# Kernel tuning notes

Hardware: AMD Instinct MI355X
Metric: run time of the kernel (lower is better)

Reference implementation:

```python
import jax, jax.numpy as jnp
import numpy as np

RES = 64
C_DIM = 64
N_BLOCKS = 4
EPS = 1e-12


def conv2d(x, w, b, pad):
    out = jax.lax.conv_general_dilated(
        x, w, window_strides=(1, 1), padding=[(pad, pad), (pad, pad)],
        dimension_numbers=('NCHW', 'OIHW', 'NCHW'))
    return out + b[None, :, None, None]


def unfold3(x):
    # F.unfold(kernel=3, padding=1): [B,C,H,W] -> [B, C*9, H*W], torch ordering (c, ki, kj)
    B, C, H, W = x.shape
    xp = jnp.pad(x, ((0, 0), (0, 0), (1, 1), (1, 1)))
    patches = jnp.stack([xp[:, :, ki:ki + H, kj:kj + W]
                         for ki in range(3) for kj in range(3)], axis=2)  # [B,C,9,H,W]
    return patches.reshape(B, C * 9, H * W)


def fold3(t, H, W):
    # F.fold(kernel=3, padding=1): sum overlapping patches back to [B,C,H,W]
    B, C9, L = t.shape
    C = C9 // 9
    t = t.reshape(B, C, 3, 3, H, W)
    out = jnp.zeros((B, C, H + 2, W + 2), t.dtype)
    for ki in range(3):
        for kj in range(3):
            out = out.at[:, :, ki:ki + H, kj:kj + W].add(t[:, :, ki, kj])
    return out[:, :, 1:H + 1, 1:W + 1]


def setup_inputs() -> dict:
    key = jax.random.key(0)
    ks = jax.random.split(key, 16)
    B, L, C = 4, RES * RES, C_DIM
    s = 0.05
    inp = {
        'c0': jax.random.normal(ks[0], (B, L, C), jnp.float32),
        'f0': jax.random.normal(ks[1], (B, L, C), jnp.float32),
        'c1': jax.random.normal(ks[2], (B, L, C), jnp.float32),
        'head_w': jax.random.normal(ks[3], (C, C, 5, 5), jnp.float32) * s,
        'head_b': jax.random.normal(ks[4], (C,), jnp.float32) * s,
        'rb_w1': jax.random.normal(ks[5], (N_BLOCKS, C, C, 3, 3), jnp.float32) * s,
        'rb_b1': jax.random.normal(ks[6], (N_BLOCKS, C), jnp.float32) * s,
        'rb_w2': jax.random.normal(ks[7], (N_BLOCKS, C, C, 3, 3), jnp.float32) * s,
        'rb_b2': jax.random.normal(ks[8], (N_BLOCKS, C), jnp.float32) * s,
        'tail_w': jax.random.normal(ks[9], (C, C, 5, 5), jnp.float32) * s,
        'tail_b': jax.random.normal(ks[10], (C,), jnp.float32) * s,
        'sq_w': jax.random.normal(ks[11], (C, 2 * C, 5, 5), jnp.float32) * s,
        'sq_b': jax.random.normal(ks[12], (C,), jnp.float32) * s,
    }
    return inp


def reference(c0, f0, c1, head_w, head_b, rb_w1, rb_b1, rb_w2, rb_b2,
              tail_w, tail_b, sq_w, sq_b):
    B, L, C = c1.shape
    H = W = RES
    c1 = c1.swapaxes(1, 2).reshape(B, C, H, W)
    c0 = c0.swapaxes(1, 2).reshape(B, C, H, W)
    f0 = f0.swapaxes(1, 2).reshape(B, C, H, W)
    Delta_c = c1 - c0

    # --- search_Trans: patch correlation + best-match texture transfer ---
    c1u = unfold3(c1)                       # [B, C9, L]
    c0u = unfold3(c0).swapaxes(1, 2)        # [B, L, C9]
    c0n = c0u / jnp.maximum(jnp.linalg.norm(c0u, axis=2, keepdims=True), EPS)
    c1n = c1u / jnp.maximum(jnp.linalg.norm(c1u, axis=1, keepdims=True), EPS)
    R = jnp.einsum('blk,bkm->blm', c0n, c1n)  # [B, L, L]
    R_star = jnp.max(R, axis=1)               # [B, L]
    R_arg = jnp.argmax(R, axis=1)              # [B, L]
    f0u = unfold3(f0)                          # [B, C9, L]
    Tu = jnp.take_along_axis(f0u, R_arg[:, None, :], axis=2)
    T = fold3(Tu, H, W) / 9.0                  # [B, C, H, W]
    S = R_star.reshape(B, 1, H, W)

    # --- residual conv stack on Delta_c ---
    x1 = conv2d(Delta_c, head_w, head_b, 2)
    x = x1
    for i in range(rb_w1.shape[0]):  # NOTE: original feeds x1 into every block
        h = jax.nn.relu(conv2d(x1, rb_w1[i], rb_b1[i], 1))
        x = conv2d(h, rb_w2[i], rb_b2[i], 1) + x1
    x = conv2d(x, tail_w, tail_b, 2)
    Delta_c_fea = x + x1

    x = conv2d(jnp.concatenate([Delta_c_fea, T], axis=1), sq_w, sq_b, 2)
    out = Delta_c_fea + x * S
    return out.reshape(B, C, L).swapaxes(1, 2)
```

## Files before the change

### kernel.cpp

```cpp
#include <hip/hip_runtime.h>
#include <hip/hip_bf16.h>


#define BATCH 4

typedef unsigned short u16;
typedef unsigned int   u32;
typedef __attribute__((ext_vector_type(8))) short short8;
typedef __attribute__((ext_vector_type(4))) float f32x4;

__device__ __forceinline__ void bsplit2(float a, float b, u32& ho, u32& lo) {
  __hip_bfloat16 ha = __float2bfloat16(a), hb = __float2bfloat16(b);
  float ra = a - __bfloat162float(ha), rb = b - __bfloat162float(hb);
  __hip_bfloat16 la = __float2bfloat16(ra), lb = __float2bfloat16(rb);
  ho = (u32)*(u16*)&ha | ((u32)*(u16*)&hb << 16);
  lo = (u32)*(u16*)&la | ((u32)*(u16*)&lb << 16);
}

__device__ __forceinline__ void gload_lds16(const void* g, void* l) {
  __builtin_amdgcn_global_load_lds((const __attribute__((address_space(1))) void*)g,
                                   (__attribute__((address_space(3))) void*)l, 16, 0, 0);
}

__global__ __launch_bounds__(256) void split_pad_kernel(const float* __restrict__ c0,
    const float* __restrict__ c1, u16* __restrict__ p0h, u16* __restrict__ p0l,
    u16* __restrict__ p1h, u16* __restrict__ p1l,
    float* __restrict__ ss0, float* __restrict__ ss1)
{
  int b = blockIdx.y, t = threadIdx.x;
  int pix = blockIdx.x * 4 + (t >> 6);
  int c = t & 63;
  int py = pix / 66, px = pix - py * 66;
  size_t d = ((size_t)b * 4356 + pix) * 64 + c;
  bool interior = (py >= 1 && py <= 64 && px >= 1 && px <= 64);
  float v0 = 0.f, v1 = 0.f;
  if (interior) {
    size_t s = (((size_t)b << 12) + ((py - 1) << 6) + (px - 1)) * 64 + c;
    v0 = c0[s]; v1 = c1[s];
  }
  __hip_bfloat16 h = __float2bfloat16(v0);
  float r = v0 - __bfloat162float(h);
  __hip_bfloat16 lo = __float2bfloat16(r);
  p0h[d] = *(u16*)&h; p0l[d] = *(u16*)&lo;
  h = __float2bfloat16(v1);
  r = v1 - __bfloat162float(h);
  lo = __float2bfloat16(r);
  p1h[d] = *(u16*)&h; p1l[d] = *(u16*)&lo;
  float s0 = v0 * v0, s1 = v1 * v1;
#pragma unroll
  for (int off = 32; off; off >>= 1) {
    s0 += __shfl_xor(s0, off);
    s1 += __shfl_xor(s1, off);
  }
  if (c == 0 && interior) {
    int sstid = (b << 12) + ((py - 1) << 6) + (px - 1);
    ss0[sstid] = s0;
    ss1[sstid] = s1;
  }
}

__global__ __launch_bounds__(256) void wprep_all(
    const float* __restrict__ hw, u16* __restrict__ whh, u16* __restrict__ whl,
    const float* __restrict__ r1, u16* __restrict__ w1h, u16* __restrict__ w1l,
    const float* __restrict__ r2, u16* __restrict__ w2h, u16* __restrict__ w2l,
    const float* __restrict__ tw, u16* __restrict__ wth, u16* __restrict__ wtl,
    const float* __restrict__ sw, u16* __restrict__ wsh, u16* __restrict__ wsl,
    const float* __restrict__ ss0, float* __restrict__ inv0)
{
  int bid = blockIdx.x;
  if (bid >= 1888) {
    int tid = (bid - 1888) * 256 + threadIdx.x;
    int b = tid >> 12, l = tid & 4095;
    int y = l >> 6, x = l & 63;
    const float* ssb = ss0 + (b << 12);
    float s = 0.f;
    for (int dy = -1; dy <= 1; ++dy) {
      int yy = y + dy; if ((unsigned)yy >= 64u) continue;
      for (int dx = -1; dx <= 1; ++dx) {
        int xx = x + dx; if ((unsigned)xx >= 64u) continue;
        s += ssb[(yy << 6) + xx];
      }
    }
    inv0[tid] = 1.f / fmaxf(sqrtf(s), 1e-12f);
    return;
  }
  const float* src; u16 *wh, *wl; int Cin, KK, n, i;
  if (bid < 400)       { src = hw; wh = whh; wl = whl; Cin = 64;  KK = 25; n = 102400; i = bid * 256; }
  else if (bid < 544)  { src = r1; wh = w1h; wl = w1l; Cin = 64;  KK = 9;  n = 36864;  i = (bid - 400) * 256; }
  else if (bid < 688)  { src = r2; wh = w2h; wl = w2l; Cin = 64;  KK = 9;  n = 36864;  i = (bid - 544) * 256; }
  else if (bid < 1088) { src = tw; wh = wth; wl = wtl; Cin = 64;  KK = 25; n = 102400; i = (bid - 688) * 256; }
  else                 { src = sw; wh = wsh; wl = wsl; Cin = 128; KK = 25; n = 204800; i = (bid - 1088) * 256; }
  i += threadIdx.x;
  if (i >= n) return;
  int per = Cin * KK;
  int cout = i / per;
  int rem = i - cout * per;
  int cin = rem / KK;
  int tap = rem - cin * KK;
  float x = src[i];
  __hip_bfloat16 h = __float2bfloat16(x);
  float r = x - __bfloat162float(h);
  __hip_bfloat16 lo = __float2bfloat16(r);
  int d = (tap * 64 + cout) * Cin + cin;
  wh[d] = *(u16*)&h;
  wl[d] = *(u16*)&lo;
}

__global__ __launch_bounds__(512) void corr_mfma(const u16* __restrict__ p0h,
    const u16* __restrict__ p0l, const u16* __restrict__ p1h, const u16* __restrict__ p1l,
    const float* __restrict__ inv0, float* __restrict__ pval, int* __restrict__ pidx)
{
  __shared__ __align__(16) u16 smem[32768];
  int mt = blockIdx.x, lt = blockIdx.y, b = blockIdx.z;
  int t = threadIdx.x;
  int lane = t & 63, w = t >> 6;
  int wa = w >> 1, wm = w & 1;
  int mat = w >> 1, half = w & 1;
  int cc = lane & 15, q = lane >> 4;
  const size_t boff = (size_t)b * 278784;
  const u16* msrc = (mat == 0) ? p0h : (mat == 1) ? p0l : (mat == 2) ? p1h : p1l;
  msrc += boff;
  const float* inv0b = inv0 + (b << 12);
  int isB = mat >> 1;

  int srow0 = lane >> 2;
  int cs_g  = (lane & 3) ^ ((lane >> 3) & 3);
  int sw    = (cc >> 1) & 3;

  const u16* gb[4];
#pragma unroll
  for (int ii = 0; ii < 4; ++ii) {
    int k = ((half * 4 + ii) << 4) + srow0;
    gb[ii] = msrc + ((((k >> 6) * 66) + (k & 63)) << 6) + (cs_g << 3);
  }

  auto stage = [&](int ssub, int sph, u16* dstbase) {
    int r = sph >> 1, hh = sph & 1;
    int ki = r / 3, kj = r - ki * 3;
    int pbr = isB ? (mt << 1) : ((lt << 3) + (ssub << 1));
    int uoff = (((pbr + ki) * 66 + kj) << 6) + (hh << 5);
#pragma unroll
    for (int ii = 0; ii < 4; ++ii)
      gload_lds16(gb[ii] + uoff, dstbase + ((half * 4 + ii) << 9));
  };

  float bval[4] = {-1e30f, -1e30f, -1e30f, -1e30f};
  int   bidx[4] = {0, 0, 0, 0};

  stage(0, 0, smem + (mat << 12));

  for (int sub = 0; sub < 4; ++sub) {
    int row0 = (lt << 9) + (sub << 7);
    f32x4 acc[2][4];
#pragma unroll
    for (int i = 0; i < 2; ++i)
#pragma unroll
      for (int j = 0; j < 4; ++j) acc[i][j] = (f32x4){0.f, 0.f, 0.f, 0.f};

    for (int ph = 0; ph < 18; ++ph) {
      int g = sub * 18 + ph;
      int nxt = g + 1;
      if (nxt < 72) {
        int np = ph + 1, ns = sub;
        if (np == 18) { np = 0; ++ns; }
        stage(ns, np, smem + ((nxt & 1) << 14) + (mat << 12));
        asm volatile("s_waitcnt vmcnt(4)" ::: "memory");
      } else {
        asm volatile("s_waitcnt vmcnt(0)" ::: "memory");
      }
      __builtin_amdgcn_s_barrier();
      __builtin_amdgcn_sched_barrier(0);
      const u16* bb = smem + ((g & 1) << 14);
      short8 afh[2], afl[2], bfh[4], bfl[4];
#pragma unroll
      for (int i = 0; i < 2; ++i) {
        int ra = (((wa << 5) + (i << 4) + cc) << 5) + ((q ^ sw) << 3);
        afh[i] = *(const short8*)(&bb[ra]);
        afl[i] = *(const short8*)(&bb[4096 + ra]);
      }
#pragma unroll
      for (int j = 0; j < 2; ++j) {
        int rb = (((wm << 6) + (j << 4) + cc) << 5) + ((q ^ sw) << 3);
        bfh[j] = *(const short8*)(&bb[8192 + rb]);
        bfl[j] = *(const short8*)(&bb[12288 + rb]);
      }
      __builtin_amdgcn_s_setprio(1);
#pragma unroll
      for (int j = 0; j < 4; ++j) {
        if (j < 2) {
          int rb = (((wm << 6) + ((j + 2) << 4) + cc) << 5) + ((q ^ sw) << 3);
          bfh[j + 2] = *(const short8*)(&bb[8192 + rb]);
          bfl[j + 2] = *(const short8*)(&bb[12288 + rb]);
        }
        __builtin_amdgcn_sched_barrier(0);
        acc[0][j] = __builtin_amdgcn_mfma_f32_16x16x32_bf16(afh[0], bfl[j], acc[0][j], 0, 0, 0);
        acc[0][j] = __builtin_amdgcn_mfma_f32_16x16x32_bf16(afl[0], bfh[j], acc[0][j], 0, 0, 0);
        acc[0][j] = __builtin_amdgcn_mfma_f32_16x16x32_bf16(afh[0], bfh[j], acc[0][j], 0, 0, 0);
        acc[1][j] = __builtin_amdgcn_mfma_f32_16x16x32_bf16(afh[1], bfl[j], acc[1][j], 0, 0, 0);
        acc[1][j] = __builtin_amdgcn_mfma_f32_16x16x32_bf16(afl[1], bfh[j], acc[1][j], 0, 0, 0);
        acc[1][j] = __builtin_amdgcn_mfma_f32_16x16x32_bf16(afh[1], bfh[j], acc[1][j], 0, 0, 0);
        __builtin_amdgcn_sched_barrier(0);
      }
      __builtin_amdgcn_s_setprio(0);
      __builtin_amdgcn_sched_barrier(0);
      __builtin_amdgcn_s_barrier();
    }
#pragma unroll
    for (int i = 0; i < 2; ++i) {
#pragma unroll
      for (int rg = 0; rg < 4; ++rg) {
        int l = row0 + (wa << 5) + (i << 4) + (q << 2) + rg;
        float sc = inv0b[l];
#pragma unroll
        for (int j = 0; j < 4; ++j) {
          float v = acc[i][j][rg] * sc;
          if (v > bval[j]) { bval[j] = v; bidx[j] = l; }
        }
      }
    }
  }

  __syncthreads();
  float* lval = (float*)smem;
  int*   lidx = (int*)((char*)smem + 8192);
  int slot = (wa << 2) + q;
#pragma unroll
  for (int j = 0; j < 4; ++j) {
    int col = (wm << 6) + (j << 4) + cc;
    lval[col * 16 + slot] = bval[j];
    lidx[col * 16 + slot] = bidx[j];
  }
  __syncthreads();
  if (t < 128) {
    float bv = -1e30f; int bi = 0x7FFFFFFF;
    for (int s = 0; s < 16; ++s) {
      float v = lval[t * 16 + s]; int id = lidx[t * 16 + s];
      if (v > bv || (v == bv && id < bi)) { bv = v; bi = id; }
    }
    size_t o = (size_t)(((b << 3) + lt) << 12) + (mt << 7) + t;
    pval[o] = bv; pidx[o] = bi;
  }
}

__global__ __launch_bounds__(256) void tgather_kernel(const float* __restrict__ f0,
    const float* __restrict__ pval, const int* __restrict__ pidx,
    const float* __restrict__ ss1, float* __restrict__ S, float* __restrict__ T)
{
  __shared__ int a3[192];
  int y = blockIdx.x, b = blockIdx.y, t = threadIdx.x;
  if (t < 192) {
    int r = t >> 6, xx = t & 63;
    int yy = y + r - 1;
    bool ok = (yy >= 0 && yy < 64);
    float bv = -1e30f; int bi = 0x7FFFFFFF;
    if (ok) {
      int m = (yy << 6) + xx;
      for (int ltv = 0; ltv < 8; ++ltv) {
        size_t o = (size_t)(((b << 3) + ltv) << 12) + m;
        float v = pval[o]; int id = pidx[o];
        if (v > bv || (v == bv && id < bi)) { bv = v; bi = id; }
      }
      if (r == 1) {
        const float* ssb = ss1 + (b << 12);
        float s = 0.f;
        for (int dy = -1; dy <= 1; ++dy) {
          int y2 = yy + dy; if ((unsigned)y2 >= 64u) continue;
          for (int dx = -1; dx <= 1; ++dx) {
            int x2 = xx + dx; if ((unsigned)x2 >= 64u) continue;
            s += ssb[(y2 << 6) + x2];
          }
        }
        S[(b << 12) + m] = bv / fmaxf(sqrtf(s), 1e-12f);
      }
    }
    a3[t] = (ok && (unsigned)bi < 4096u) ? bi : 0;
  }
  __syncthreads();
  int c = t & 63, pg = t >> 6;
  for (int it = 0; it < 16; ++it) {
    int px = pg + (it << 2);
    float sum = 0.f;
#pragma unroll
    for (int ki = 0; ki < 3; ++ki) {
      int yn = y + 1 - ki;
      if (yn < 0 || yn >= 64) continue;
#pragma unroll
      for (int kj = 0; kj < 3; ++kj) {
        int xn = px + 1 - kj;
        if (xn < 0 || xn >= 64) continue;
        int p = a3[((2 - ki) << 6) + xn];
        int sy = (p >> 6) + ki - 1, sx = (p & 63) + kj - 1;
        if (sy >= 0 && sy < 64 && sx >= 0 && sx < 64)
          sum += f0[((((size_t)b << 12) + (sy << 6) + sx) << 6) + c];
      }
    }
    T[((((size_t)b << 12) + (y << 6) + px)) * 64 + c] = sum * (1.f / 9.f);
  }
}

template<int KS, int CINCH>
__global__ __launch_bounds__(256) void conv_mfma(const float* __restrict__ in0,
    const float* __restrict__ in1, const u16* __restrict__ whp, const u16* __restrict__ wlp,
    const float* __restrict__ bias, float* __restrict__ outp,
    const float* __restrict__ res, const float* __restrict__ smul, int dorelu, int dm)
{
  constexpr int P = KS / 2;
  constexpr int CIN = CINCH * 32;
  constexpr int NKH = CINCH / 2;
  constexpr int NIT = KS * KS * NKH;
  constexpr int AST = 72;
  __shared__ __align__(16) u16 Ah[2][32 * AST], Al[2][32 * AST];
  __shared__ __align__(16) u16 Bh[2][64 * AST], Bl[2][64 * AST];
  int tile = blockIdx.x, b = blockIdx.y;
  int t = threadIdx.x;
  int lane = t & 63, w = t >> 6;
  int wpx = w >> 1, wm = w & 1;
  int cc = lane & 15, q = lane >> 4;
  int ty = tile >> 1, txb = (tile & 1) << 5;
  const size_t abase = (size_t)b << 12;
  f32x4 acc[2];
  acc[0] = (f32x4){0.f, 0.f, 0.f, 0.f};
  acc[1] = (f32x4){0.f, 0.f, 0.f, 0.f};

  uint4 rg[8];
  int arow = t >> 2, acs = t & 3;
  int tb = t - 128;
  int brow = tb >> 1, bhalf = tb & 1;

  auto issue_loads = [&](int itn) {
    int tapn = (NKH == 1) ? itn : (itn >> 1);
    int kh   = (NKH == 1) ? 0 : (itn & 1);
    int ki = tapn / KS, kj = tapn - ki * KS;
    if (t < 128) {
#pragma unroll
      for (int k = 0; k < 8; ++k) rg[k] = make_uint4(0u, 0u, 0u, 0u);
      int iy = ty + ki - P;
      int ix = txb + arow + kj - P;
      if ((unsigned)iy < 64u && (unsigned)ix < 64u) {
        size_t base = (abase + (iy << 6) + ix) << 6;
        int cg = kh * 64 + acs * 16;
        if (dm) {
#pragma unroll
          for (int k = 0; k < 4; ++k) {
            rg[k]     = *(const uint4*)(in0 + base + cg + 4 * k);
            rg[4 + k] = *(const uint4*)(in1 + base + cg + 4 * k);
          }
        } else {
          const float* sp = (CINCH == 4 && kh == 1) ? (in1 + base + (cg - 64))
                                                    : (in0 + base + cg);
#pragma unroll
          for (int k = 0; k < 4; ++k) rg[k] = *(const uint4*)(sp + 4 * k);
        }
      }
    } else {
      size_t so = (size_t)(tapn * 64 + brow) * CIN + kh * 64 + bhalf * 32;
#pragma unroll
      for (int k = 0; k < 4; ++k) {
        rg[k]     = *(const uint4*)&whp[so + 8 * k];
        rg[4 + k] = *(const uint4*)&wlp[so + 8 * k];
      }
    }
  };

  auto write_lds = [&](int cur) {
    if (t < 128) {
      float v[16];
      if (dm) {
#pragma unroll
        for (int k = 0; k < 4; ++k)
#pragma unroll
          for (int e = 0; e < 4; ++e)
            v[k * 4 + e] = __uint_as_float((&rg[4 + k].x)[e]) - __uint_as_float((&rg[k].x)[e]);
      } else {
#pragma unroll
        for (int k = 0; k < 4; ++k)
#pragma unroll
          for (int e = 0; e < 4; ++e)
            v[k * 4 + e] = __uint_as_float((&rg[k].x)[e]);
      }
      uint4 uh0, ul0, uh1, ul1;
      bsplit2(v[0], v[1], uh0.x, ul0.x);
      bsplit2(v[2], v[3], uh0.y, ul0.y);
      bsplit2(v[4], v[5], uh0.z, ul0.z);
      bsplit2(v[6], v[7], uh0.w, ul0.w);
      bsplit2(v[8], v[9], uh1.x, ul1.x);
      bsplit2(v[10], v[11], uh1.y, ul1.y);
      bsplit2(v[12], v[13], uh1.z, ul1.z);
      bsplit2(v[14], v[15], uh1.w, ul1.w);
      int o = arow * AST + acs * 16;
      *(uint4*)&Ah[cur][o]     = uh0;
      *(uint4*)&Ah[cur][o + 8] = uh1;
      *(uint4*)&Al[cur][o]     = ul0;
      *(uint4*)&Al[cur][o + 8] = ul1;
    } else {
      int o = brow * AST + bhalf * 32;
#pragma unroll
      for (int k = 0; k < 4; ++k) {
        *(uint4*)&Bh[cur][o + 8 * k] = rg[k];
        *(uint4*)&Bl[cur][o + 8 * k] = rg[4 + k];
      }
    }
  };

  issue_loads(0);
  for (int it = 0; it < NIT; ++it) {
    int cur = it & 1;
    write_lds(cur);
    if (it + 1 < NIT) issue_loads(it + 1);
    asm volatile("s_waitcnt lgkmcnt(0)" ::: "memory");
    __builtin_amdgcn_s_barrier();
    __builtin_amdgcn_sched_barrier(0);
    short8 afh[2], afl[2], bfh[2][2], bfl[2][2];
#pragma unroll
    for (int ks = 0; ks < 2; ++ks) {
      int ra = ((wpx << 4) + cc) * AST + ks * 32 + (q << 3);
      afh[ks] = *(const short8*)&Ah[cur][ra];
      afl[ks] = *(const short8*)&Al[cur][ra];
#pragma unroll
      for (int j = 0; j < 2; ++j) {
        int rb = ((wm << 5) + (j << 4) + cc) * AST + ks * 32 + (q << 3);
        bfh[j][ks] = *(const short8*)&Bh[cur][rb];
        bfl[j][ks] = *(const short8*)&Bl[cur][rb];
      }
    }
#pragma unroll
    for (int ks = 0; ks < 2; ++ks) {
      acc[0] = __builtin_amdgcn_mfma_f32_16x16x32_bf16(afh[ks], bfl[0][ks], acc[0], 0, 0, 0);
      acc[1] = __builtin_amdgcn_mfma_f32_16x16x32_bf16(afh[ks], bfl[1][ks], acc[1], 0, 0, 0);
      acc[0] = __builtin_amdgcn_mfma_f32_16x16x32_bf16(afl[ks], bfh[0][ks], acc[0], 0, 0, 0);
      acc[1] = __builtin_amdgcn_mfma_f32_16x16x32_bf16(afl[ks], bfh[1][ks], acc[1], 0, 0, 0);
      acc[0] = __builtin_amdgcn_mfma_f32_16x16x32_bf16(afh[ks], bfh[0][ks], acc[0], 0, 0, 0);
      acc[1] = __builtin_amdgcn_mfma_f32_16x16x32_bf16(afh[ks], bfh[1][ks], acc[1], 0, 0, 0);
    }
  }
#pragma unroll
  for (int rgi = 0; rgi < 4; ++rgi) {
    int p = (ty << 6) + txb + (wpx << 4) + (q << 2) + rgi;
#pragma unroll
    for (int j = 0; j < 2; ++j) {
      int cout = (wm << 5) + (j << 4) + cc;
      float v = acc[j][rgi] + bias[cout];
      if (dorelu) v = fmaxf(v, 0.f);
      size_t oi = ((abase + p) << 6) + cout;
      if (smul) v = res[oi] + v * smul[abase + p];
      else if (res) v += res[oi];
      outp[oi] = v;
    }
  }
}

extern "C" void kernel_launch(void* const* d_in, const int* in_sizes, int n_in,
                              void* d_out, int out_size, void* d_ws, size_t ws_size,
                              hipStream_t stream)
{
  (void)in_sizes; (void)n_in; (void)out_size; (void)ws_size;
  const float* c0     = (const float*)d_in[0];
  const float* f0     = (const float*)d_in[1];
  const float* c1     = (const float*)d_in[2];
  const float* head_w = (const float*)d_in[3];
  const float* head_b = (const float*)d_in[4];
  const float* rb_w1  = (const float*)d_in[5];
  const float* rb_b1  = (const float*)d_in[6];
  const float* rb_w2  = (const float*)d_in[7];
  const float* rb_b2  = (const float*)d_in[8];
  const float* tail_w = (const float*)d_in[9];
  const float* tail_b = (const float*)d_in[10];
  const float* sq_w   = (const float*)d_in[11];
  const float* sq_b   = (const float*)d_in[12];
  float* out = (float*)d_out;
  char* ws = (char*)d_ws;

  const size_t OFF_SS0  = 0;
  const size_t OFF_SS1  = 65536;
  const size_t OFF_INV0 = 131072;
  const size_t OFF_S    = 262144;
  const size_t OFF_PVAL = 393216;
  const size_t OFF_PIDX = 917504;
  const size_t OFF_WHH  = 1441792;
  const size_t OFF_WHL  = 1646592;
  const size_t OFF_W1H  = 1851392;
  const size_t OFF_W1L  = 1925120;
  const size_t OFF_W2H  = 1998848;
  const size_t OFF_W2L  = 2072576;
  const size_t OFF_WTH  = 2146304;
  const size_t OFF_WTL  = 2351104;
  const size_t OFF_WSH  = 2555904;
  const size_t OFF_WSL  = 2965504;
  const size_t OFF_P0H  = 3375104;
  const size_t OFF_P0L  = OFF_P0H + 2230272;
  const size_t OFF_P1H  = OFF_P0L + 2230272;
  const size_t OFF_P1L  = OFF_P1H + 2230272;
  const size_t OFF_SA   = 3375104;
  const size_t OFF_SB   = 7569408;
  const size_t OFF_SC   = 11763712;

  float* ss0  = (float*)(ws + OFF_SS0);
  float* ss1  = (float*)(ws + OFF_SS1);
  float* inv0 = (float*)(ws + OFF_INV0);
  float* Sbuf = (float*)(ws + OFF_S);
  float* pval = (float*)(ws + OFF_PVAL);
  int*   pidx = (int*)(ws + OFF_PIDX);
  u16* whh = (u16*)(ws + OFF_WHH); u16* whl = (u16*)(ws + OFF_WHL);
  u16* w1h = (u16*)(ws + OFF_W1H); u16* w1l = (u16*)(ws + OFF_W1L);
  u16* w2h = (u16*)(ws + OFF_W2H); u16* w2l = (u16*)(ws + OFF_W2L);
  u16* wth = (u16*)(ws + OFF_WTH); u16* wtl = (u16*)(ws + OFF_WTL);
  u16* wsh = (u16*)(ws + OFF_WSH); u16* wsl = (u16*)(ws + OFF_WSL);
  u16* p0h = (u16*)(ws + OFF_P0H); u16* p0l = (u16*)(ws + OFF_P0L);
  u16* p1h = (u16*)(ws + OFF_P1H); u16* p1l = (u16*)(ws + OFF_P1L);
  float* x1  = (float*)(ws + OFF_SA);
  float* Tb  = (float*)(ws + OFF_SA);
  float* hb  = (float*)(ws + OFF_SB);
  float* dcf = (float*)(ws + OFF_SB);
  float* xb  = (float*)(ws + OFF_SC);

  dim3 b256(256);
  split_pad_kernel<<<dim3(1089, BATCH), b256, 0, stream>>>(c0, c1, p0h, p0l, p1h, p1l, ss0, ss1);
  wprep_all<<<dim3(1952), b256, 0, stream>>>(head_w, whh, whl,
      rb_w1 + 110592, w1h, w1l, rb_w2 + 110592, w2h, w2l,
      tail_w, wth, wtl, sq_w, wsh, wsl, ss0, inv0);

  corr_mfma<<<dim3(32, 8, BATCH), dim3(512), 0, stream>>>(p0h, p0l, p1h, p1l, inv0, pval, pidx);

  dim3 cgrid(128, BATCH);
  conv_mfma<5, 2><<<cgrid, b256, 0, stream>>>(c0, c1, whh, whl, head_b, x1, nullptr, nullptr, 0, 1);
  conv_mfma<3, 2><<<cgrid, b256, 0, stream>>>(x1, nullptr, w1h, w1l, rb_b1 + 192, hb, nullptr, nullptr, 1, 0);
  conv_mfma<3, 2><<<cgrid, b256, 0, stream>>>(hb, nullptr, w2h, w2l, rb_b2 + 192, xb, x1, nullptr, 0, 0);
  conv_mfma<5, 2><<<cgrid, b256, 0, stream>>>(xb, nullptr, wth, wtl, tail_b, dcf, x1, nullptr, 0, 0);

  tgather_kernel<<<dim3(64, BATCH), b256, 0, stream>>>(f0, pval, pidx, ss1, Sbuf, Tb);
  conv_mfma<5, 4><<<cgrid, b256, 0, stream>>>(dcf, Tb, wsh, wsl, sq_b, out, dcf, Sbuf, 0, 0);
}
```

Measured before the change: 495.4 us.

## Fuse split/wprep launches and co-schedule head conv with correlation kernel

Merges the padding/bf16-split kernel and the weight-prep kernel into one launch, and moves the inverse-norm computation into the correlation kernel's LDS prologue. When the workspace is large enough, the head 5x5 conv is interleaved as extra blocks inside the correlation launch, with idle waves matching its barrier count. The aim is to cut launch count and let the small conv fill idle CUs during the correlation. In exchange it adds blocks (and shared memory) to the correlation grid, and barrier matching between the two paths is fragile.

```diff
diff --git a/kernel.cpp b/kernel.cpp
--- a/kernel.cpp
+++ b/kernel.cpp
@@ -22,75 +22,59 @@
                                    (__attribute__((address_space(3))) void*)l, 16, 0, 0);
 }
 
-__global__ __launch_bounds__(256) void split_pad_kernel(const float* __restrict__ c0,
-    const float* __restrict__ c1, u16* __restrict__ p0h, u16* __restrict__ p0l,
+__global__ __launch_bounds__(256) void split_wprep_kernel(
+    const float* __restrict__ c0, const float* __restrict__ c1,
+    u16* __restrict__ p0h, u16* __restrict__ p0l,
     u16* __restrict__ p1h, u16* __restrict__ p1l,
-    float* __restrict__ ss0, float* __restrict__ ss1)
-{
-  int b = blockIdx.y, t = threadIdx.x;
-  int pix = blockIdx.x * 4 + (t >> 6);
-  int c = t & 63;
-  int py = pix / 66, px = pix - py * 66;
-  size_t d = ((size_t)b * 4356 + pix) * 64 + c;
-  bool interior = (py >= 1 && py <= 64 && px >= 1 && px <= 64);
-  float v0 = 0.f, v1 = 0.f;
-  if (interior) {
-    size_t s = (((size_t)b << 12) + ((py - 1) << 6) + (px - 1)) * 64 + c;
-    v0 = c0[s]; v1 = c1[s];
-  }
-  __hip_bfloat16 h = __float2bfloat16(v0);
-  float r = v0 - __bfloat162float(h);
-  __hip_bfloat16 lo = __float2bfloat16(r);
-  p0h[d] = *(u16*)&h; p0l[d] = *(u16*)&lo;
-  h = __float2bfloat16(v1);
-  r = v1 - __bfloat162float(h);
-  lo = __float2bfloat16(r);
-  p1h[d] = *(u16*)&h; p1l[d] = *(u16*)&lo;
-  float s0 = v0 * v0, s1 = v1 * v1;
-#pragma unroll
-  for (int off = 32; off; off >>= 1) {
-    s0 += __shfl_xor(s0, off);
-    s1 += __shfl_xor(s1, off);
-  }
-  if (c == 0 && interior) {
-    int sstid = (b << 12) + ((py - 1) << 6) + (px - 1);
-    ss0[sstid] = s0;
-    ss1[sstid] = s1;
-  }
-}
-
-__global__ __launch_bounds__(256) void wprep_all(
+    float* __restrict__ ss0, float* __restrict__ ss1,
     const float* __restrict__ hw, u16* __restrict__ whh, u16* __restrict__ whl,
     const float* __restrict__ r1, u16* __restrict__ w1h, u16* __restrict__ w1l,
     const float* __restrict__ r2, u16* __restrict__ w2h, u16* __restrict__ w2l,
     const float* __restrict__ tw, u16* __restrict__ wth, u16* __restrict__ wtl,
-    const float* __restrict__ sw, u16* __restrict__ wsh, u16* __restrict__ wsl,
-    const float* __restrict__ ss0, float* __restrict__ inv0)
+    const float* __restrict__ sw, u16* __restrict__ wsh, u16* __restrict__ wsl)
 {
-  int bid = blockIdx.x;
-  if (bid >= 1888) {
-    int tid = (bid - 1888) * 256 + threadIdx.x;
-    int b = tid >> 12, l = tid & 4095;
-    int y = l >> 6, x = l & 63;
-    const float* ssb = ss0 + (b << 12);
-    float s = 0.f;
-    for (int dy = -1; dy <= 1; ++dy) {
-      int yy = y + dy; if ((unsigned)yy >= 64u) continue;
-      for (int dx = -1; dx <= 1; ++dx) {
-        int xx = x + dx; if ((unsigned)xx >= 64u) continue;
-        s += ssb[(yy << 6) + xx];
-      }
-    }
-    inv0[tid] = 1.f / fmaxf(sqrtf(s), 1e-12f);
+  int bid = blockIdx.x, t = threadIdx.x;
+  if (bid < 4356) {
+    int b = bid & 3;
+    int pix = (bid >> 2) * 4 + (t >> 6);
+    int c = t & 63;
+    int py = pix / 66, px = pix - py * 66;
+    size_t d = ((size_t)b * 4356 + pix) * 64 + c;
+    bool interior = (py >= 1 && py <= 64 && px >= 1 && px <= 64);
+    float v0 = 0.f, v1 = 0.f;
+    if (interior) {
+      size_t s = (((size_t)b << 12) + ((py - 1) << 6) + (px - 1)) * 64 + c;
+      v0 = c0[s]; v1 = c1[s];
+    }
+    __hip_bfloat16 h = __float2bfloat16(v0);
+    float r = v0 - __bfloat162float(h);
+    __hip_bfloat16 lo = __float2bfloat16(r);
+    p0h[d] = *(u16*)&h; p0l[d] = *(u16*)&lo;
+    h = __float2bfloat16(v1);
+    r = v1 - __bfloat162float(h);
+    lo = __float2bfloat16(r);
+    p1h[d] = *(u16*)&h; p1l[d] = *(u16*)&lo;
+    float s0 = v0 * v0, s1 = v1 * v1;
+#pragma unroll
+    for (int off = 32; off; off >>= 1) {
+      s0 += __shfl_xor(s0, off);
+      s1 += __shfl_xor(s1, off);
+    }
+    if (c == 0 && interior) {
+      int sstid = (b << 12) + ((py - 1) << 6) + (px - 1);
+      ss0[sstid] = s0;
+      ss1[sstid] = s1;
+    }
     return;
   }
+  int wb = bid - 4356;
   const float* src; u16 *wh, *wl; int Cin, KK, n, i;
-  if (bid < 400)       { src = hw; wh = whh; wl = whl; Cin = 64;  KK = 25; n = 102400; i = bid * 256; }
-  else if (bid < 544)  { src = r1; wh = w1h; wl = w1l; Cin = 64;  KK = 9;  n = 36864;  i = (bid - 400) * 256; }
-  else if (bid < 688)  { src = r2; wh = w2h; wl = w2l; Cin = 64;  KK = 9;  n = 36864;  i = (bid - 544) * 256; }
-  else if (bid < 1088) { src = tw; wh = wth; wl = wtl; Cin = 64;  KK = 25; n = 102400; i = (bid - 688) * 256; }
-  else                 { src = sw; wh = wsh; wl = wsl; Cin = 128; KK = 25; n = 204800; i = (bid - 1088) * 256; }
-  i += threadIdx.x;
+  if (wb < 400)       { src = hw; wh = whh; wl = whl; Cin = 64;  KK = 25; n = 102400; i = wb * 256; }
+  else if (wb < 544)  { src = r1; wh = w1h; wl = w1l; Cin = 64;  KK = 9;  n = 36864;  i = (wb - 400) * 256; }
+  else if (wb < 688)  { src = r2; wh = w2h; wl = w2l; Cin = 64;  KK = 9;  n = 36864;  i = (wb - 544) * 256; }
+  else if (wb < 1088) { src = tw; wh = wth; wl = wtl; Cin = 64;  KK = 25; n = 102400; i = (wb - 688) * 256; }
+  else                { src = sw; wh = wsh; wl = wsl; Cin = 128; KK = 25; n = 204800; i = (wb - 1088) * 256; }
+  i += t;
   if (i >= n) return;
   int per = Cin * KK;
   int cout = i / per;
@@ -106,13 +90,199 @@
   wl[d] = *(u16*)&lo;
 }
 
-__global__ __launch_bounds__(512) void corr_mfma(const u16* __restrict__ p0h,
+template<int KS, int CINCH>
+__device__ __forceinline__ void conv_body(u16* __restrict__ lds, int tile, int b, int t,
+    const float* __restrict__ in0, const float* __restrict__ in1,
+    const u16* __restrict__ whp, const u16* __restrict__ wlp,
+    const float* __restrict__ bias, float* __restrict__ outp,
+    const float* __restrict__ res, const float* __restrict__ smul, int dorelu, int dm)
+{
+  constexpr int P = KS / 2;
+  constexpr int CIN = CINCH * 32;
+  constexpr int NKH = CINCH / 2;
+  constexpr int NIT = KS * KS * NKH;
+  constexpr int AST = 72;
+  u16* Ah = lds;
+  u16* Al = lds + 4608;
+  u16* Bh = lds + 9216;
+  u16* Bl = lds + 18432;
+  int lane = t & 63, w = t >> 6;
+  int wpx = w >> 1, wm = w & 1;
+  int cc = lane & 15, q = lane >> 4;
+  int ty = tile >> 1, txb = (tile & 1) << 5;
+  const size_t abase = (size_t)b << 12;
+  f32x4 acc[2];
+  acc[0] = (f32x4){0.f, 0.f, 0.f, 0.f};
+  acc[1] = (f32x4){0.f, 0.f, 0.f, 0.f};
+
+  uint4 rg[8];
+  int arow = t >> 2, acs = t & 3;
+  int tb = t - 128;
+  int brow = tb >> 1, bhalf = tb & 1;
+
+  auto issue_loads = [&](int itn) {
+    int tapn = (NKH == 1) ? itn : (itn >> 1);
+    int kh   = (NKH == 1) ? 0 : (itn & 1);
+    int ki = tapn / KS, kj = tapn - ki * KS;
+    if (t < 128) {
+#pragma unroll
+      for (int k = 0; k < 8; ++k) rg[k] = make_uint4(0u, 0u, 0u, 0u);
+      int iy = ty + ki - P;
+      int ix = txb + arow + kj - P;
+      if ((unsigned)iy < 64u && (unsigned)ix < 64u) {
+        size_t base = (abase + (iy << 6) + ix) << 6;
+        int cg = kh * 64 + acs * 16;
+        if (dm) {
+#pragma unroll
+          for (int k = 0; k < 4; ++k) {
+            rg[k]     = *(const uint4*)(in0 + base + cg + 4 * k);
+            rg[4 + k] = *(const uint4*)(in1 + base + cg + 4 * k);
+          }
+        } else {
+          const float* sp = (CINCH == 4 && kh == 1) ? (in1 + base + (cg - 64))
+                                                    : (in0 + base + cg);
+#pragma unroll
+          for (int k = 0; k < 4; ++k) rg[k] = *(const uint4*)(sp + 4 * k);
+        }
+      }
+    } else {
+      size_t so = (size_t)(tapn * 64 + brow) * CIN + kh * 64 + bhalf * 32;
+#pragma unroll
+      for (int k = 0; k < 4; ++k) {
+        rg[k]     = *(const uint4*)&whp[so + 8 * k];
+        rg[4 + k] = *(const uint4*)&wlp[so + 8 * k];
+      }
+    }
+  };
+
+  auto write_lds = [&](int cur) {
+    if (t < 128) {
+      float v[16];
+      if (dm) {
+#pragma unroll
+        for (int k = 0; k < 4; ++k)
+#pragma unroll
+          for (int e = 0; e < 4; ++e)
+            v[k * 4 + e] = __uint_as_float((&rg[4 + k].x)[e]) - __uint_as_float((&rg[k].x)[e]);
+      } else {
+#pragma unroll
+        for (int k = 0; k < 4; ++k)
+#pragma unroll
+          for (int e = 0; e < 4; ++e)
+            v[k * 4 + e] = __uint_as_float((&rg[k].x)[e]);
+      }
+      uint4 uh0, ul0, uh1, ul1;
+      bsplit2(v[0], v[1], uh0.x, ul0.x);
+      bsplit2(v[2], v[3], uh0.y, ul0.y);
+      bsplit2(v[4], v[5], uh0.z, ul0.z);
+      bsplit2(v[6], v[7], uh0.w, ul0.w);
+      bsplit2(v[8], v[9], uh1.x, ul1.x);
+      bsplit2(v[10], v[11], uh1.y, ul1.y);
+      bsplit2(v[12], v[13], uh1.z, ul1.z);
+      bsplit2(v[14], v[15], uh1.w, ul1.w);
+      int o = cur * 2304 + arow * AST + acs * 16;
+      *(uint4*)&Ah[o]     = uh0;
+      *(uint4*)&Ah[o + 8] = uh1;
+      *(uint4*)&Al[o]     = ul0;
+      *(uint4*)&Al[o + 8] = ul1;
+    } else {
+      int o = cur * 4608 + brow * AST + bhalf * 32;
+#pragma unroll
+      for (int k = 0; k < 4; ++k) {
+        *(uint4*)&Bh[o + 8 * k] = rg[k];
+        *(uint4*)&Bl[o + 8 * k] = rg[4 + k];
+      }
+    }
+  };
+
+  issue_loads(0);
+  for (int it = 0; it < NIT; ++it) {
+    int cur = it & 1;
+    write_lds(cur);
+    if (it + 1 < NIT) issue_loads(it + 1);
+    asm volatile("s_waitcnt lgkmcnt(0)" ::: "memory");
+    __builtin_amdgcn_s_barrier();
+    __builtin_amdgcn_sched_barrier(0);
+    short8 afh[2], afl[2], bfh[2][2], bfl[2][2];
+#pragma unroll
+    for (int ks = 0; ks < 2; ++ks) {
+      int ra = cur * 2304 + ((wpx << 4) + cc) * AST + ks * 32 + (q << 3);
+      afh[ks] = *(const short8*)&Ah[ra];
+      afl[ks] = *(const short8*)&Al[ra];
+#pragma unroll
+      for (int j = 0; j < 2; ++j) {
+        int rb = cur * 4608 + ((wm << 5) + (j << 4) + cc) * AST + ks * 32 + (q << 3);
+        bfh[j][ks] = *(const short8*)&Bh[rb];
+        bfl[j][ks] = *(const short8*)&Bl[rb];
+      }
+    }
+#pragma unroll
+    for (int ks = 0; ks < 2; ++ks) {
+      acc[0] = __builtin_amdgcn_mfma_f32_16x16x32_bf16(afh[ks], bfl[0][ks], acc[0], 0, 0, 0);
+      acc[1] = __builtin_amdgcn_mfma_f32_16x16x32_bf16(afh[ks], bfl[1][ks], acc[1], 0, 0, 0);
+      acc[0] = __builtin_amdgcn_mfma_f32_16x16x32_bf16(afl[ks], bfh[0][ks], acc[0], 0, 0, 0);
+      acc[1] = __builtin_amdgcn_mfma_f32_16x16x32_bf16(afl[ks], bfh[1][ks], acc[1], 0, 0, 0);
+      acc[0] = __builtin_amdgcn_mfma_f32_16x16x32_bf16(afh[ks], bfh[0][ks], acc[0], 0, 0, 0);
+      acc[1] = __builtin_amdgcn_mfma_f32_16x16x32_bf16(afh[ks], bfh[1][ks], acc[1], 0, 0, 0);
+    }
+  }
+#pragma unroll
+  for (int rgi = 0; rgi < 4; ++rgi) {
+    int p = (ty << 6) + txb + (wpx << 4) + (q << 2) + rgi;
+#pragma unroll
+    for (int j = 0; j < 2; ++j) {
+      int cout = (wm << 5) + (j << 4) + cc;
+      float v = acc[j][rgi] + bias[cout];
+      if (dorelu) v = fmaxf(v, 0.f);
+      size_t oi = ((abase + p) << 6) + cout;
+      if (smul) v = res[oi] + v * smul[abase + p];
+      else if (res) v += res[oi];
+      outp[oi] = v;
+    }
+  }
+}
+
+template<int KS, int CINCH>
+__global__ __launch_bounds__(256) void conv_mfma(const float* __restrict__ in0,
+    const float* __restrict__ in1, const u16* __restrict__ whp, const u16* __restrict__ wlp,
+    const float* __restrict__ bias, float* __restrict__ outp,
+    const float* __restrict__ res, const float* __restrict__ smul, int dorelu, int dm)
+{
+  __shared__ __align__(16) u16 lds[27648];
+  conv_body<KS, CINCH>(lds, blockIdx.x, blockIdx.y, threadIdx.x,
+                       in0, in1, whp, wlp, bias, outp, res, smul, dorelu, dm);
+}
+
+__global__ __launch_bounds__(512) void corr_conv1(const u16* __restrict__ p0h,
     const u16* __restrict__ p0l, const u16* __restrict__ p1h, const u16* __restrict__ p1l,
-    const float* __restrict__ inv0, float* __restrict__ pval, int* __restrict__ pidx)
+    const float* __restrict__ ss0, float* __restrict__ pval, int* __restrict__ pidx,
+    const float* __restrict__ c0, const float* __restrict__ c1,
+    const u16* __restrict__ whh, const u16* __restrict__ whl,
+    const float* __restrict__ head_b, float* __restrict__ x1, int nconv)
 {
-  __shared__ __align__(16) u16 smem[32768];
-  int mt = blockIdx.x, lt = blockIdx.y, b = blockIdx.z;
-  int t = threadIdx.x;
+  __shared__ __align__(16) u16 raw16[33792];
+  int bid = blockIdx.x, t = threadIdx.x;
+  int kid;
+  if (nconv) {
+    int r3 = bid % 3, d3 = bid / 3;
+    if (r3 == 2) {
+      int w = t >> 6;
+      if (w < 4) {
+        conv_body<5, 2>(raw16, d3 & 127, d3 >> 7, t, c0, c1, whh, whl, head_b,
+                        x1, nullptr, nullptr, 0, 1);
+      } else {
+        for (int it = 0; it < 25; ++it) __builtin_amdgcn_s_barrier();
+      }
+      return;
+    }
+    kid = d3 * 2 + r3;
+  } else {
+    kid = bid;
+  }
+
+  u16* smem = raw16;
+  float* linv = (float*)(raw16 + 32768);
+  int mt = kid & 31, lt = (kid >> 5) & 7, b = kid >> 8;
   int lane = t & 63, w = t >> 6;
   int wa = w >> 1, wm = w & 1;
   int mat = w >> 1, half = w & 1;
@@ -120,8 +290,22 @@
   const size_t boff = (size_t)b * 278784;
   const u16* msrc = (mat == 0) ? p0h : (mat == 1) ? p0l : (mat == 2) ? p1h : p1l;
   msrc += boff;
-  const float* inv0b = inv0 + (b << 12);
   int isB = mat >> 1;
+
+  {
+    const float* ssb = ss0 + (b << 12);
+    int l = (lt << 9) + t;
+    int y = l >> 6, x = l & 63;
+    float s = 0.f;
+    for (int dy = -1; dy <= 1; ++dy) {
+      int yy = y + dy; if ((unsigned)yy >= 64u) continue;
+      for (int dx = -1; dx <= 1; ++dx) {
+        int xx = x + dx; if ((unsigned)xx >= 64u) continue;
+        s += ssb[(yy << 6) + xx];
+      }
+    }
+    linv[t] = 1.f / fmaxf(sqrtf(s), 1e-12f);
+  }
 
   int srow0 = lane >> 2;
   int cs_g  = (lane & 3) ^ ((lane >> 3) & 3);
@@ -150,7 +334,6 @@
   stage(0, 0, smem + (mat << 12));
 
   for (int sub = 0; sub < 4; ++sub) {
-    int row0 = (lt << 9) + (sub << 7);
     f32x4 acc[2][4];
 #pragma unroll
     for (int i = 0; i < 2; ++i)
@@ -209,8 +392,9 @@
     for (int i = 0; i < 2; ++i) {
 #pragma unroll
       for (int rg = 0; rg < 4; ++rg) {
-        int l = row0 + (wa << 5) + (i << 4) + (q << 2) + rg;
-        float sc = inv0b[l];
+        int rl = (sub << 7) + (wa << 5) + (i << 4) + (q << 2) + rg;
+        float sc = linv[rl];
+        int l = (lt << 9) + rl;
 #pragma unroll
         for (int j = 0; j < 4; ++j) {
           float v = acc[i][j][rg] * sc;
@@ -298,162 +482,11 @@
   }
 }
 
-template<int KS, int CINCH>
-__global__ __launch_bounds__(256) void conv_mfma(const float* __restrict__ in0,
-    const float* __restrict__ in1, const u16* __restrict__ whp, const u16* __restrict__ wlp,
-    const float* __restrict__ bias, float* __restrict__ outp,
-    const float* __restrict__ res, const float* __restrict__ smul, int dorelu, int dm)
-{
-  constexpr int P = KS / 2;
-  constexpr int CIN = CINCH * 32;
-  constexpr int NKH = CINCH / 2;
-  constexpr int NIT = KS * KS * NKH;
-  constexpr int AST = 72;
-  __shared__ __align__(16) u16 Ah[2][32 * AST], Al[2][32 * AST];
-  __shared__ __align__(16) u16 Bh[2][64 * AST], Bl[2][64 * AST];
-  int tile = blockIdx.x, b = blockIdx.y;
-  int t = threadIdx.x;
-  int lane = t & 63, w = t >> 6;
-  int wpx = w >> 1, wm = w & 1;
-  int cc = lane & 15, q = lane >> 4;
-  int ty = tile >> 1, txb = (tile & 1) << 5;
-  const size_t abase = (size_t)b << 12;
-  f32x4 acc[2];
-  acc[0] = (f32x4){0.f, 0.f, 0.f, 0.f};
-  acc[1] = (f32x4){0.f, 0.f, 0.f, 0.f};
-
-  uint4 rg[8];
-  int arow = t >> 2, acs = t & 3;
-  int tb = t - 128;
-  int brow = tb >> 1, bhalf = tb & 1;
-
-  auto issue_loads = [&](int itn) {
-    int tapn = (NKH == 1) ? itn : (itn >> 1);
-    int kh   = (NKH == 1) ? 0 : (itn & 1);
-    int ki = tapn / KS, kj = tapn - ki * KS;
-    if (t < 128) {
-#pragma unroll
-      for (int k = 0; k < 8; ++k) rg[k] = make_uint4(0u, 0u, 0u, 0u);
-      int iy = ty + ki - P;
-      int ix = txb + arow + kj - P;
-      if ((unsigned)iy < 64u && (unsigned)ix < 64u) {
-        size_t base = (abase + (iy << 6) + ix) << 6;
-        int cg = kh * 64 + acs * 16;
-        if (dm) {
-#pragma unroll
-          for (int k = 0; k < 4; ++k) {
-            rg[k]     = *(const uint4*)(in0 + base + cg + 4 * k);
-            rg[4 + k] = *(const uint4*)(in1 + base + cg + 4 * k);
-          }
-        } else {
-          const float* sp = (CINCH == 4 && kh == 1) ? (in1 + base + (cg - 64))
-                                                    : (in0 + base + cg);
-#pragma unroll
-          for (int k = 0; k < 4; ++k) rg[k] = *(const uint4*)(sp + 4 * k);
-        }
-      }
-    } else {
-      size_t so = (size_t)(tapn * 64 + brow) * CIN + kh * 64 + bhalf * 32;
-#pragma unroll
-      for (int k = 0; k < 4; ++k) {
-        rg[k]     = *(const uint4*)&whp[so + 8 * k];
-        rg[4 + k] = *(const uint4*)&wlp[so + 8 * k];
-      }
-    }
-  };
-
-  auto write_lds = [&](int cur) {
-    if (t < 128) {
-      float v[16];
-      if (dm) {
-#pragma unroll
-        for (int k = 0; k < 4; ++k)
-#pragma unroll
-          for (int e = 0; e < 4; ++e)
-            v[k * 4 + e] = __uint_as_float((&rg[4 + k].x)[e]) - __uint_as_float((&rg[k].x)[e]);
-      } else {
-#pragma unroll
-        for (int k = 0; k < 4; ++k)
-#pragma unroll
-          for (int e = 0; e < 4; ++e)
-            v[k * 4 + e] = __uint_as_float((&rg[k].x)[e]);
-      }
-      uint4 uh0, ul0, uh1, ul1;
-      bsplit2(v[0], v[1], uh0.x, ul0.x);
-      bsplit2(v[2], v[3], uh0.y, ul0.y);
-      bsplit2(v[4], v[5], uh0.z, ul0.z);
-      bsplit2(v[6], v[7], uh0.w, ul0.w);
-      bsplit2(v[8], v[9], uh1.x, ul1.x);
-      bsplit2(v[10], v[11], uh1.y, ul1.y);
-      bsplit2(v[12], v[13], uh1.z, ul1.z);
-      bsplit2(v[14], v[15], uh1.w, ul1.w);
-      int o = arow * AST + acs * 16;
-      *(uint4*)&Ah[cur][o]     = uh0;
-      *(uint4*)&Ah[cur][o + 8] = uh1;
-      *(uint4*)&Al[cur][o]     = ul0;
-      *(uint4*)&Al[cur][o + 8] = ul1;
-    } else {
-      int o = brow * AST + bhalf * 32;
-#pragma unroll
-      for (int k = 0; k < 4; ++k) {
-        *(uint4*)&Bh[cur][o + 8 * k] = rg[k];
-        *(uint4*)&Bl[cur][o + 8 * k] = rg[4 + k];
-      }
-    }
-  };
-
-  issue_loads(0);
-  for (int it = 0; it < NIT; ++it) {
-    int cur = it & 1;
-    write_lds(cur);
-    if (it + 1 < NIT) issue_loads(it + 1);
-    asm volatile("s_waitcnt lgkmcnt(0)" ::: "memory");
-    __builtin_amdgcn_s_barrier();
-    __builtin_amdgcn_sched_barrier(0);
-    short8 afh[2], afl[2], bfh[2][2], bfl[2][2];
-#pragma unroll
-    for (int ks = 0; ks < 2; ++ks) {
-      int ra = ((wpx << 4) + cc) * AST + ks * 32 + (q << 3);
-      afh[ks] = *(const short8*)&Ah[cur][ra];
-      afl[ks] = *(const short8*)&Al[cur][ra];
-#pragma unroll
-      for (int j = 0; j < 2; ++j) {
-        int rb = ((wm << 5) + (j << 4) + cc) * AST + ks * 32 + (q << 3);
-        bfh[j][ks] = *(const short8*)&Bh[cur][rb];
-        bfl[j][ks] = *(const short8*)&Bl[cur][rb];
-      }
-    }
-#pragma unroll
-    for (int ks = 0; ks < 2; ++ks) {
-      acc[0] = __builtin_amdgcn_mfma_f32_16x16x32_bf16(afh[ks], bfl[0][ks], acc[0], 0, 0, 0);
-      acc[1] = __builtin_amdgcn_mfma_f32_16x16x32_bf16(afh[ks], bfl[1][ks], acc[1], 0, 0, 0);
-      acc[0] = __builtin_amdgcn_mfma_f32_16x16x32_bf16(afl[ks], bfh[0][ks], acc[0], 0, 0, 0);
-      acc[1] = __builtin_amdgcn_mfma_f32_16x16x32_bf16(afl[ks], bfh[1][ks], acc[1], 0, 0, 0);
-      acc[0] = __builtin_amdgcn_mfma_f32_16x16x32_bf16(afh[ks], bfh[0][ks], acc[0], 0, 0, 0);
-      acc[1] = __builtin_amdgcn_mfma_f32_16x16x32_bf16(afh[ks], bfh[1][ks], acc[1], 0, 0, 0);
-    }
-  }
-#pragma unroll
-  for (int rgi = 0; rgi < 4; ++rgi) {
-    int p = (ty << 6) + txb + (wpx << 4) + (q << 2) + rgi;
-#pragma unroll
-    for (int j = 0; j < 2; ++j) {
-      int cout = (wm << 5) + (j << 4) + cc;
-      float v = acc[j][rgi] + bias[cout];
-      if (dorelu) v = fmaxf(v, 0.f);
-      size_t oi = ((abase + p) << 6) + cout;
-      if (smul) v = res[oi] + v * smul[abase + p];
-      else if (res) v += res[oi];
-      outp[oi] = v;
-    }
-  }
-}
-
 extern "C" void kernel_launch(void* const* d_in, const int* in_sizes, int n_in,
                               void* d_out, int out_size, void* d_ws, size_t ws_size,
                               hipStream_t stream)
 {
-  (void)in_sizes; (void)n_in; (void)out_size; (void)ws_size;
+  (void)in_sizes; (void)n_in; (void)out_size;
   const float* c0     = (const float*)d_in[0];
   const float* f0     = (const float*)d_in[1];
   const float* c1     = (const float*)d_in[2];
@@ -472,7 +505,6 @@
 
   const size_t OFF_SS0  = 0;
   const size_t OFF_SS1  = 65536;
-  const size_t OFF_INV0 = 131072;
   const size_t OFF_S    = 262144;
   const size_t OFF_PVAL = 393216;
   const size_t OFF_PIDX = 917504;
@@ -490,13 +522,10 @@
   const size_t OFF_P0L  = OFF_P0H + 2230272;
   const size_t OFF_P1H  = OFF_P0L + 2230272;
   const size_t OFF_P1L  = OFF_P1H + 2230272;
-  const size_t OFF_SA   = 3375104;
-  const size_t OFF_SB   = 7569408;
-  const size_t OFF_SC   = 11763712;
+  const size_t OFF_X1B  = 12296192;
 
   float* ss0  = (float*)(ws + OFF_SS0);
   float* ss1  = (float*)(ws + OFF_SS1);
-  float* inv0 = (float*)(ws + OFF_INV0);
   float* Sbuf = (float*)(ws + OFF_S);
   float* pval = (float*)(ws + OFF_PVAL);
   int*   pidx = (int*)(ws + OFF_PIDX);
@@ -507,22 +536,39 @@
   u16* wsh = (u16*)(ws + OFF_WSH); u16* wsl = (u16*)(ws + OFF_WSL);
   u16* p0h = (u16*)(ws + OFF_P0H); u16* p0l = (u16*)(ws + OFF_P0L);
   u16* p1h = (u16*)(ws + OFF_P1H); u16* p1l = (u16*)(ws + OFF_P1L);
-  float* x1  = (float*)(ws + OFF_SA);
-  float* Tb  = (float*)(ws + OFF_SA);
-  float* hb  = (float*)(ws + OFF_SB);
-  float* dcf = (float*)(ws + OFF_SB);
-  float* xb  = (float*)(ws + OFF_SC);
+
+  bool big = ws_size >= (OFF_X1B + 4194304);
+  float *x1, *hb, *xb, *dcf, *Tb;
+  if (big) {
+    x1  = (float*)(ws + OFF_X1B);
+    hb  = (float*)(ws + OFF_P0H);
+    xb  = (float*)(ws + 7569408);
+    dcf = (float*)(ws + OFF_P0H);
+    Tb  = (float*)(ws + 7569408);
+  } else {
+    x1  = (float*)(ws + OFF_P0H);
+    hb  = (float*)(ws + 7569408);
+    xb  = (float*)(ws + 11763712);
+    dcf = (float*)(ws + 7569408);
+    Tb  = (float*)(ws + OFF_P0H);
+  }
 
   dim3 b256(256);
-  split_pad_kernel<<<dim3(1089, BATCH), b256, 0, stream>>>(c0, c1, p0h, p0l, p1h, p1l, ss0, ss1);
-  wprep_all<<<dim3(1952), b256, 0, stream>>>(head_w, whh, whl,
-      rb_w1 + 110592, w1h, w1l, rb_w2 + 110592, w2h, w2l,
-      tail_w, wth, wtl, sq_w, wsh, wsl, ss0, inv0);
-
-  corr_mfma<<<dim3(32, 8, BATCH), dim3(512), 0, stream>>>(p0h, p0l, p1h, p1l, inv0, pval, pidx);
+  split_wprep_kernel<<<dim3(6244), b256, 0, stream>>>(c0, c1, p0h, p0l, p1h, p1l,
+      ss0, ss1, head_w, whh, whl, rb_w1 + 110592, w1h, w1l, rb_w2 + 110592, w2h, w2l,
+      tail_w, wth, wtl, sq_w, wsh, wsl);
 
   dim3 cgrid(128, BATCH);
-  conv_mfma<5, 2><<<cgrid, b256, 0, stream>>>(c0, c1, whh, whl, head_b, x1, nullptr, nullptr, 0, 1);
+  if (big) {
+    corr_conv1<<<dim3(1536), dim3(512), 0, stream>>>(p0h, p0l, p1h, p1l, ss0,
+        pval, pidx, c0, c1, whh, whl, head_b, x1, 512);
+  } else {
+    corr_conv1<<<dim3(1024), dim3(512), 0, stream>>>(p0h, p0l, p1h, p1l, ss0,
+        pval, pidx, c0, c1, whh, whl, head_b, x1, 0);
+    conv_mfma<5, 2><<<cgrid, b256, 0, stream>>>(c0, c1, whh, whl, head_b, x1,
+        nullptr, nullptr, 0, 1);
+  }
+
   conv_mfma<3, 2><<<cgrid, b256, 0, stream>>>(x1, nullptr, w1h, w1l, rb_b1 + 192, hb, nullptr, nullptr, 1, 0);
   conv_mfma<3, 2><<<cgrid, b256, 0, stream>>>(hb, nullptr, w2h, w2l, rb_b2 + 192, xb, x1, nullptr, 0, 0);
   conv_mfma<5, 2><<<cgrid, b256, 0, stream>>>(xb, nullptr, wth, wtl, tail_b, dcf, x1, nullptr, 0, 0);
```

After: 502.9 us. Within noise of the previous version (+1.5%).
